# Kernel optimization log

Hardware: AMD Instinct MI355X
Metric: run time of the kernel (lower is better)

Reference implementation:

```python
import jax, jax.numpy as jnp
import numpy as np

B, L, C = 16, 2048, 128
FACTOR = 5
EPS = 1e-5


def setup_inputs() -> dict:
    key = jax.random.key(0)
    ks = jax.random.split(key, 16)
    U = min(FACTOR * int(np.ceil(np.log(L))), L)  # U_part == u == 40 for L=2048
    inp = {"x": jax.random.normal(ks[0], (B, L, C), jnp.float32)}
    scalar_names = ["Wq", "bq", "Wk", "bk", "Wv", "bv", "Wo", "bo", "w1", "b1", "w2", "b2"]
    for i, n in enumerate(scalar_names):
        inp[n] = jax.random.normal(ks[i + 1], (1,), jnp.float32) * 0.5
    inp["g1"] = jnp.ones((1,), jnp.float32)
    inp["beta1"] = jnp.zeros((1,), jnp.float32)
    inp["g2"] = jnp.ones((1,), jnp.float32)
    inp["beta2"] = jnp.zeros((1,), jnp.float32)
    # ProbAttention's random key-sampling indices (torch.randint(L_K, (L_Q, sample_k)))
    inp["index_sample"] = jax.random.randint(ks[14], (L, U), 0, L, dtype=jnp.int32)
    return inp


def _layernorm(x, g, b):
    # norm_dims=2 with d_model=1: normalize jointly over (seq_len, 1) == seq axis here
    m = x.mean(-1, keepdims=True)
    v = x.var(-1, keepdims=True)
    return (x - m) * jax.lax.rsqrt(v + EPS) * g + b


def reference(x, Wq, bq, Wk, bk, Wv, bv, Wo, bo, w1, b1, w2, b2,
              g1, beta1, g2, beta2, index_sample):
    U = index_sample.shape[1]  # sample_k == n_top (L_Q == L_K)
    batch_idx = jnp.arange(B)[:, None]

    def chan(xc):  # xc: [B, L] one channel, d_model=1 squeezed (H=1, D=1 -> scale=1)
        q = xc * Wq + bq
        k = xc * Wk + bk
        v = xc * Wv + bv
        # sparse measurement: sample U keys per query
        K_s = k[:, index_sample]                      # [B, L, U]
        QK = q[:, :, None] * K_s                      # [B, L, U]
        M = QK.max(-1) - QK.sum(-1) / L               # [B, L]
        _, M_top = jax.lax.top_k(M, U)                # [B, U] top-u query indices
        Qr = jnp.take_along_axis(q, M_top, axis=1)    # [B, U]
        scores = Qr[:, :, None] * k[:, None, :]       # [B, U, L], scale = 1/sqrt(1)
        attn = jax.nn.softmax(scores, axis=-1)
        upd = jnp.einsum('bul,bl->bu', attn, v)       # [B, U]
        # initial context = mean of V (mask_flag=False), updated at top queries
        ctx = jnp.broadcast_to(v.mean(1, keepdims=True), xc.shape)
        ctx = ctx.at[batch_idx, M_top].set(upd)       # [B, L]
        new_x = ctx * Wo + bo                          # out_projection
        x1 = _layernorm(xc + new_x, g1, beta1)
        y = jax.nn.gelu(x1 * w1 + b1, approximate=False)  # conv1 (1x1, 1->1) + gelu
        y = y * w2 + b2                                    # conv2 (1x1, 1->1)
        return _layernorm(x1 + y, g2, beta2)

    # all cfg.d_model encoder layers share one weight set -> vmap over channels
    return jax.vmap(chan, in_axes=2, out_axes=2)(x)  # [B, L, C]
```

## Files before the change

kernel.cpp:

```cpp
#include <hip/hip_runtime.h>
#include <math.h>

#define LL 2048
#define CC 128
#define BB 16
#define UU 40
#define NT 256
#define NW 4
#define EPSF 1e-5f

__device__ __forceinline__ float waveSum(float v) {
#pragma unroll
    for (int off = 1; off < 64; off <<= 1) v += __shfl_xor(v, off, 64);
    return v;
}
__device__ __forceinline__ float waveMax(float v) {
#pragma unroll
    for (int off = 1; off < 64; off <<= 1) v = fmaxf(v, __shfl_xor(v, off, 64));
    return v;
}
__device__ __forceinline__ float waveMin(float v) {
#pragma unroll
    for (int off = 1; off < 64; off <<= 1) v = fminf(v, __shfl_xor(v, off, 64));
    return v;
}
__device__ __forceinline__ float blockSum(float v, volatile float* scr) {
    v = waveSum(v);
    const int lane = threadIdx.x & 63, wid = threadIdx.x >> 6;
    __syncthreads();
    if (lane == 0) scr[wid] = v;
    __syncthreads();
    return scr[0] + scr[1] + scr[2] + scr[3];
}
__device__ __forceinline__ float blockMax(float v, volatile float* scr) {
    v = waveMax(v);
    const int lane = threadIdx.x & 63, wid = threadIdx.x >> 6;
    __syncthreads();
    if (lane == 0) scr[wid] = v;
    __syncthreads();
    return fmaxf(fmaxf(scr[0], scr[1]), fmaxf(scr[2], scr[3]));
}
__device__ __forceinline__ float blockMin(float v, volatile float* scr) {
    v = waveMin(v);
    const int lane = threadIdx.x & 63, wid = threadIdx.x >> 6;
    __syncthreads();
    if (lane == 0) scr[wid] = v;
    __syncthreads();
    return fminf(fminf(scr[0], scr[1]), fminf(scr[2], scr[3]));
}

__global__ __launch_bounds__(256) void transpose_dual(
    const float* __restrict__ x,  float* __restrict__ xT,
    const float* __restrict__ M,  float* __restrict__ MT) {
    __shared__ float t[32][33];
    const int z  = blockIdx.z;
    const int b  = (z < BB) ? z : (z - BB);
    const float* in  = (z < BB) ? x  : M;
    float* outp      = (z < BB) ? xT : MT;
    const int c0 = blockIdx.x * 32, l0 = blockIdx.y * 32;
    const int lx = threadIdx.x, ly = threadIdx.y;
    const float* base = in + ((size_t)b * LL + l0) * CC + c0;
#pragma unroll
    for (int i = 0; i < 4; ++i) t[ly + i * 8][lx] = base[(size_t)(ly + i * 8) * CC + lx];
    __syncthreads();
    float* obase = outp + ((size_t)b * CC + c0) * LL + l0;
#pragma unroll
    for (int i = 0; i < 4; ++i) obase[(size_t)(ly + i * 8) * LL + lx] = t[lx][ly + i * 8];
}
__global__ __launch_bounds__(256) void transpose_out(const float* __restrict__ in,
                                                     float* __restrict__ outp) {
    __shared__ float t[32][33];
    const int b  = blockIdx.z;
    const int l0 = blockIdx.x * 32, c0 = blockIdx.y * 32;
    const int lx = threadIdx.x, ly = threadIdx.y;
    const float* base = in + ((size_t)b * CC + c0) * LL + l0;
#pragma unroll
    for (int i = 0; i < 4; ++i) t[ly + i * 8][lx] = base[(size_t)(ly + i * 8) * LL + lx];
    __syncthreads();
    float* obase = outp + ((size_t)b * LL + l0) * CC + c0;
#pragma unroll
    for (int i = 0; i < 4; ++i) obase[(size_t)(ly + i * 8) * CC + lx] = t[lx][ly + i * 8];
}

__global__ __launch_bounds__(256) void agg_kernel(
    const float* __restrict__ x, const int* __restrict__ idx,
    const float* __restrict__ gWq, const float* __restrict__ gbq,
    const float* __restrict__ gWk, const float* __restrict__ gbk,
    float* __restrict__ M)
{
    __shared__ int s_idx[8 * UU];
    const int tid = threadIdx.x;
    const int g   = blockIdx.x;
    const int b   = ((g & 7) << 1) | ((g >> 3) & 1);
    const int l0  = (g >> 4) * 8;
    if (tid < 256)          s_idx[tid]       = idx[l0 * UU + tid];
    if (tid < 8 * UU - 256) s_idx[256 + tid] = idx[l0 * UU + 256 + tid];
    __syncthreads();

    const int s = tid & 31;
    const int r = tid >> 5;
    const int l = l0 + r;
    const float Wq = *gWq, bq = *gbq, Wk = *gWk, bk = *gbk;

    const float4* xb = (const float4*)(x + (size_t)b * LL * CC);
    float4 xo4 = xb[(size_t)l * 32 + s];
    float xo[4] = {xo4.x, xo4.y, xo4.z, xo4.w};

    float  mx[4] = {-3.4e38f, -3.4e38f, -3.4e38f, -3.4e38f};
    float  mn[4] = { 3.4e38f,  3.4e38f,  3.4e38f,  3.4e38f};
    double sm[4] = {0.0, 0.0, 0.0, 0.0};
    const int* rowp = &s_idx[r * UU];
#pragma unroll 8
    for (int u = 0; u < UU; ++u) {
        const int i = rowp[u];
        float4 xv = xb[(size_t)i * 32 + s];
        float xa[4] = {xv.x, xv.y, xv.z, xv.w};
#pragma unroll
        for (int t = 0; t < 4; ++t) {
            mx[t] = fmaxf(mx[t], xa[t]);
            mn[t] = fminf(mn[t], xa[t]);
            sm[t] += (double)xa[t];
        }
    }
    float mo[4];
#pragma unroll
    for (int t = 0; t < 4; ++t) {
        const float xH = (Wk >= 0.f) ? mx[t] : mn[t];
        const float xL = (Wk >= 0.f) ? mn[t] : mx[t];
        const float kH = __fadd_rn(__fmul_rn(xH, Wk), bk);
        const float kL = __fadd_rn(__fmul_rn(xL, Wk), bk);
        const float q  = __fadd_rn(__fmul_rn(xo[t], Wq), bq);
        const float t1 = __fmul_rn(q, (q >= 0.f) ? kH : kL);
        const double ks = (double)Wk * sm[t] + 40.0 * (double)bk;
        const float t2 = (float)(((double)q * ks) * (1.0 / 2048.0));
        mo[t] = __fsub_rn(t1, t2);
    }
    float4 Mo = make_float4(mo[0], mo[1], mo[2], mo[3]);
    ((float4*)(M + ((size_t)b * LL + l) * CC))[s] = Mo;
}

__global__ __launch_bounds__(NT) void rowBC(
    const float* __restrict__ xT,
    float* MoT,
    const float* __restrict__ gWq, const float* __restrict__ gbq,
    const float* __restrict__ gWk, const float* __restrict__ gbk,
    const float* __restrict__ gWv, const float* __restrict__ gbv,
    const float* __restrict__ gWo, const float* __restrict__ gbo,
    const float* __restrict__ gw1, const float* __restrict__ gb1,
    const float* __restrict__ gw2, const float* __restrict__ gb2,
    const float* __restrict__ gg1, const float* __restrict__ gbe1,
    const float* __restrict__ gg2, const float* __restrict__ gbe2)
{
    const int tid = threadIdx.x;
    const int ln  = tid & 63;
    const int wid = tid >> 6;
    const int r   = blockIdx.x * 4 + wid;

    __shared__ __align__(16) float s_ctx[4][LL];
    __shared__ int s_top[4][UU];

    const float Wq = *gWq, bq = *gbq, Wk = *gWk, bk = *gbk;
    const float Wv = *gWv, bv = *gbv, Wo = *gWo, bo = *gbo;
    const float w1 = *gw1, b1 = *gb1, w2 = *gw2, b2 = *gb2;
    const float g1 = *gg1, be1 = *gbe1, g2 = *gg2, be2 = *gbe2;

    const float*  xrow  = xT + (size_t)r * LL;
    const float4* xrow4 = (const float4*)xrow;
    float* Mrow = MoT + (size_t)r * LL;
    const float4* mrow4 = (const float4*)Mrow;
    float4* orow4 = (float4*)Mrow;
    float4* lds4  = (float4*)s_ctx[wid];

    float4 mv[8];
#pragma unroll
    for (int m = 0; m < 8; ++m) mv[m] = mrow4[ln + m * 64];

    float bvv = -3.4e38f; int bii = LL + 1;
#pragma unroll
    for (int m = 0; m < 8; ++m) {
        const int l0 = 4 * (ln + 64 * m);
        if (mv[m].x > bvv) { bvv = mv[m].x; bii = l0; }
        if (mv[m].y > bvv) { bvv = mv[m].y; bii = l0 + 1; }
        if (mv[m].z > bvv) { bvv = mv[m].z; bii = l0 + 2; }
        if (mv[m].w > bvv) { bvv = mv[m].w; bii = l0 + 3; }
    }
    for (int t = 0; t < UU; ++t) {
        float rv = bvv; int ri = bii;
#pragma unroll
        for (int off = 1; off < 64; off <<= 1) {
            float ov = __shfl_xor(rv, off, 64);
            int   oi = __shfl_xor(ri, off, 64);
            if (ov > rv || (ov == rv && oi < ri)) { rv = ov; ri = oi; }
        }
        if (ln == 0) s_top[wid][t] = ri;
        if (bii == ri) {
#pragma unroll
            for (int m = 0; m < 8; ++m) {
                const int l0 = 4 * (ln + 64 * m);
                if (l0     == ri) mv[m].x = -3.4e38f;
                if (l0 + 1 == ri) mv[m].y = -3.4e38f;
                if (l0 + 2 == ri) mv[m].z = -3.4e38f;
                if (l0 + 3 == ri) mv[m].w = -3.4e38f;
            }
            bvv = -3.4e38f; bii = LL + 1;
#pragma unroll
            for (int m = 0; m < 8; ++m) {
                const int l0 = 4 * (ln + 64 * m);
                if (mv[m].x > bvv) { bvv = mv[m].x; bii = l0; }
                if (mv[m].y > bvv) { bvv = mv[m].y; bii = l0 + 1; }
                if (mv[m].z > bvv) { bvv = mv[m].z; bii = l0 + 2; }
                if (mv[m].w > bvv) { bvv = mv[m].w; bii = l0 + 3; }
            }
        }
    }

    float4 xc[8];
    float vsum = 0.f, xmx = -3.4e38f, xmn = 3.4e38f;
#pragma unroll
    for (int m = 0; m < 8; ++m) {
        float4 xv = xrow4[ln + m * 64];
        xc[m] = xv;
        vsum += __fadd_rn(__fmul_rn(xv.x, Wv), bv) + __fadd_rn(__fmul_rn(xv.y, Wv), bv)
              + __fadd_rn(__fmul_rn(xv.z, Wv), bv) + __fadd_rn(__fmul_rn(xv.w, Wv), bv);
        xmx = fmaxf(xmx, fmaxf(fmaxf(xv.x, xv.y), fmaxf(xv.z, xv.w)));
        xmn = fminf(xmn, fminf(fminf(xv.x, xv.y), fminf(xv.z, xv.w)));
    }
    vsum = waveSum(vsum);
    xmx  = waveMax(xmx);
    xmn  = waveMin(xmn);
    const float vmean = vsum * (1.f / (float)LL);
    const float kmx = __fadd_rn(__fmul_rn((Wk >= 0.f) ? xmx : xmn, Wk), bk);
    const float kmn = __fadd_rn(__fmul_rn((Wk >= 0.f) ? xmn : xmx, Wk), bk);

#pragma unroll
    for (int m = 0; m < 8; ++m)
        lds4[ln + m * 64] = make_float4(vmean, vmean, vmean, vmean);

    for (int g = 0; g < UU / 4; ++g) {
        int p[4]; float qp[4], sm[4];
#pragma unroll
        for (int q = 0; q < 4; ++q) {
            p[q] = s_top[wid][g * 4 + q];
            const float xq = xrow[p[q]];
            qp[q] = __fadd_rn(__fmul_rn(xq, Wq), bq);
            sm[q] = (qp[q] >= 0.f) ? __fmul_rn(qp[q], kmx) : __fmul_rn(qp[q], kmn);
        }
        float se[4] = {0.f, 0.f, 0.f, 0.f};
        float sx[4] = {0.f, 0.f, 0.f, 0.f};
#pragma unroll
        for (int m = 0; m < 8; ++m) {
            float4 x4 = xc[m];
            float4 k4;
            k4.x = __fadd_rn(__fmul_rn(x4.x, Wk), bk);
            k4.y = __fadd_rn(__fmul_rn(x4.y, Wk), bk);
            k4.z = __fadd_rn(__fmul_rn(x4.z, Wk), bk);
            k4.w = __fadd_rn(__fmul_rn(x4.w, Wk), bk);
#pragma unroll
            for (int q = 0; q < 4; ++q) {
                float e;
                e = __expf(fmaf(qp[q], k4.x, -sm[q])); se[q] += e; sx[q] = fmaf(e, x4.x, sx[q]);
                e = __expf(fmaf(qp[q], k4.y, -sm[q])); se[q] += e; sx[q] = fmaf(e, x4.y, sx[q]);
                e = __expf(fmaf(qp[q], k4.z, -sm[q])); se[q] += e; sx[q] = fmaf(e, x4.z, sx[q]);
                e = __expf(fmaf(qp[q], k4.w, -sm[q])); se[q] += e; sx[q] = fmaf(e, x4.w, sx[q]);
            }
        }
#pragma unroll
        for (int q = 0; q < 4; ++q) {
            const float seA = waveSum(se[q]);
            const float sxA = waveSum(sx[q]);
            const float upd = (Wv * sxA + bv * seA) / seA;
            if (ln == 0) s_ctx[wid][p[q]] = upd;
        }
    }

    float4 tt[8];
    float lsum = 0.f;
#pragma unroll
    for (int m = 0; m < 8; ++m) {
        float4 cx = lds4[ln + m * 64], xv = xc[m], tv;
        tv.x = xv.x + __fadd_rn(__fmul_rn(cx.x, Wo), bo);
        tv.y = xv.y + __fadd_rn(__fmul_rn(cx.y, Wo), bo);
        tv.z = xv.z + __fadd_rn(__fmul_rn(cx.z, Wo), bo);
        tv.w = xv.w + __fadd_rn(__fmul_rn(cx.w, Wo), bo);
        tt[m] = tv;
        lsum += tv.x + tv.y + tv.z + tv.w;
    }
    const float mean1 = waveSum(lsum) * (1.f / (float)LL);
    float lss = 0.f;
#pragma unroll
    for (int m = 0; m < 8; ++m) {
        float4 tv = tt[m];
        float d0 = tv.x - mean1, d1 = tv.y - mean1, d2 = tv.z - mean1, d3 = tv.w - mean1;
        lss += d0 * d0 + d1 * d1 + d2 * d2 + d3 * d3;
    }
    const float var1 = waveSum(lss) * (1.f / (float)LL);
    const float rs1 = rsqrtf(var1 + EPSF);

    float lsum2 = 0.f;
#pragma unroll
    for (int m = 0; m < 8; ++m) {
        float4 tv = tt[m], zz;
        {
            float x1 = (tv.x - mean1) * rs1 * g1 + be1;
            float a = x1 * w1 + b1;
            float y = 0.5f * a * (1.f + erff(a * 0.70710678118654752f));
            zz.x = x1 + (y * w2 + b2);
        }
        {
            float x1 = (tv.y - mean1) * rs1 * g1 + be1;
            float a = x1 * w1 + b1;
            float y = 0.5f * a * (1.f + erff(a * 0.70710678118654752f));
            zz.y = x1 + (y * w2 + b2);
        }
        {
            float x1 = (tv.z - mean1) * rs1 * g1 + be1;
            float a = x1 * w1 + b1;
            float y = 0.5f * a * (1.f + erff(a * 0.70710678118654752f));
            zz.z = x1 + (y * w2 + b2);
        }
        {
            float x1 = (tv.w - mean1) * rs1 * g1 + be1;
            float a = x1 * w1 + b1;
            float y = 0.5f * a * (1.f + erff(a * 0.70710678118654752f));
            zz.w = x1 + (y * w2 + b2);
        }
        tt[m] = zz;
        lsum2 += zz.x + zz.y + zz.z + zz.w;
    }
    const float mean2 = waveSum(lsum2) * (1.f / (float)LL);
    float lss2 = 0.f;
#pragma unroll
    for (int m = 0; m < 8; ++m) {
        float4 zz = tt[m];
        float d0 = zz.x - mean2, d1 = zz.y - mean2, d2 = zz.z - mean2, d3 = zz.w - mean2;
        lss2 += d0 * d0 + d1 * d1 + d2 * d2 + d3 * d3;
    }
    const float var2 = waveSum(lss2) * (1.f / (float)LL);
    const float rs2 = rsqrtf(var2 + EPSF);

#pragma unroll
    for (int m = 0; m < 8; ++m) {
        float4 zz = tt[m], oo;
        oo.x = (zz.x - mean2) * rs2 * g2 + be2;
        oo.y = (zz.y - mean2) * rs2 * g2 + be2;
        oo.z = (zz.z - mean2) * rs2 * g2 + be2;
        oo.w = (zz.w - mean2) * rs2 * g2 + be2;
        orow4[ln + m * 64] = oo;
    }
}

__global__ __launch_bounds__(NT) void informer_fallback(
    const float* __restrict__ xin,
    const float* __restrict__ gWq, const float* __restrict__ gbq,
    const float* __restrict__ gWk, const float* __restrict__ gbk,
    const float* __restrict__ gWv, const float* __restrict__ gbv,
    const float* __restrict__ gWo, const float* __restrict__ gbo,
    const float* __restrict__ gw1, const float* __restrict__ gb1,
    const float* __restrict__ gw2, const float* __restrict__ gb2,
    const float* __restrict__ gg1, const float* __restrict__ gbe1,
    const float* __restrict__ gg2, const float* __restrict__ gbe2,
    const int* __restrict__ idx,
    float* __restrict__ outp)
{
    const int tid  = threadIdx.x;
    const int lane = tid & 63;
    const int wid  = tid >> 6;
    const int blk  = blockIdx.x;
    const int b    = blk >> 7;
    const int c    = blk & (CC - 1);

    __shared__ float  s_xc[LL];
    __shared__ float  s_kc[LL];
    __shared__ float  s_v[LL];
    __shared__ float  s_red[NW];
    __shared__ double s_cv[NW * UU];
    __shared__ int    s_ci[NW * UU];
    __shared__ int    s_top[UU];
    __shared__ float  s_upd[UU];

    const float Wq = *gWq, bq = *gbq, Wk = *gWk, bk = *gbk;
    const float Wv = *gWv, bv = *gbv, Wo = *gWo, bo = *gbo;
    const float w1 = *gw1, b1 = *gb1, w2 = *gw2, b2 = *gb2;
    const float g1 = *gg1, be1 = *gbe1, g2 = *gg2, be2 = *gbe2;

    const float* xrow = xin + (size_t)b * LL * CC + c;
    float* orow = outp + (size_t)b * LL * CC + c;

    float vsum = 0.f, kmn = 3.4e38f, kmx = -3.4e38f;
    for (int l = tid; l < LL; l += NT) {
        float xv = xrow[(size_t)l * CC];
        s_xc[l] = xv;
        float kvv = __fadd_rn(__fmul_rn(xv, Wk), bk);
        float vvv = __fadd_rn(__fmul_rn(xv, Wv), bv);
        s_kc[l] = kvv;
        s_v[l] = vvv;
        vsum += vvv;
        kmn = fminf(kmn, kvv);
        kmx = fmaxf(kmx, kvv);
    }
    const float vmean  = blockSum(vsum, s_red) * (1.f / (float)LL);
    const float kmxAll = blockMax(kmx, s_red);
    const float kmnAll = blockMin(kmn, s_red);

    double mloc[8];
#pragma unroll
    for (int j = 0; j < 8; ++j) {
        const int l = tid + NT * j;
        const float qv = __fadd_rn(__fmul_rn(s_xc[l], Wq), bq);
        const double qd = (double)qv;
        const int* row = idx + l * UU;
        float kmaxs = -3.4e38f, kmins = 3.4e38f;
        double ssum = 0.0;
#pragma unroll 8
        for (int u = 0; u < UU; ++u) {
            float kvv = s_kc[row[u]];
            kmaxs = fmaxf(kmaxs, kvv);
            kmins = fminf(kmins, kvv);
            ssum += (double)kvv;
        }
        double qmax = (qd >= 0.0) ? qd * (double)kmaxs : qd * (double)kmins;
        mloc[j] = qmax - qd * ssum * (1.0 / (double)LL);
    }

    double wbv = mloc[0]; int wbi = tid;
#pragma unroll
    for (int j = 1; j < 8; ++j)
        if (mloc[j] > wbv) { wbv = mloc[j]; wbi = tid + NT * j; }

    for (int t = 0; t < UU; ++t) {
        double rv = wbv; int ri = wbi;
#pragma unroll
        for (int off = 1; off < 64; off <<= 1) {
            double ov = __shfl_xor(rv, off, 64);
            int    oi = __shfl_xor(ri, off, 64);
            if (ov > rv || (ov == rv && oi < ri)) { rv = ov; ri = oi; }
        }
        if (lane == 0) { s_cv[wid * UU + t] = rv; s_ci[wid * UU + t] = ri; }
        if (wbi == ri) {
#pragma unroll
            for (int j = 0; j < 8; ++j) if ((tid + NT * j) == ri) mloc[j] = -1e300;
            wbv = mloc[0]; wbi = tid;
#pragma unroll
            for (int j = 1; j < 8; ++j)
                if (mloc[j] > wbv) { wbv = mloc[j]; wbi = tid + NT * j; }
        }
    }
    __syncthreads();

    if (wid == 0) {
        double c0v = s_cv[lane], c1v = s_cv[lane + 64];
        int    c0i = s_ci[lane], c1i = s_ci[lane + 64];
        double c2v = (lane < 32) ? s_cv[lane + 128] : -1e300;
        int    c2i = (lane < 32) ? s_ci[lane + 128] : (LL + 1);
        for (int t = 0; t < UU; ++t) {
            double rv = c0v; int ri = c0i;
            if (c1v > rv || (c1v == rv && c1i < ri)) { rv = c1v; ri = c1i; }
            if (c2v > rv || (c2v == rv && c2i < ri)) { rv = c2v; ri = c2i; }
#pragma unroll
            for (int off = 1; off < 64; off <<= 1) {
                double ov = __shfl_xor(rv, off, 64);
                int    oi = __shfl_xor(ri, off, 64);
                if (ov > rv || (ov == rv && oi < ri)) { rv = ov; ri = oi; }
            }
            if (lane == 0) s_top[t] = ri;
            if (c0i == ri) c0v = -1e300;
            else if (c1i == ri) c1v = -1e300;
            else if (c2i == ri) c2v = -1e300;
        }
    }
    __syncthreads();

    for (int r = 0; r < UU / NW; ++r) {
        const int u = r * NW + wid;
        const int p = s_top[u];
        const float qp = __fadd_rn(__fmul_rn(s_xc[p], Wq), bq);
        const float smax = (qp >= 0.f) ? qp * kmxAll : qp * kmnAll;
        float se = 0.f, sev = 0.f;
        for (int l = lane; l < LL; l += 64) {
            float e = __expf(qp * s_kc[l] - smax);
            se += e;
            sev = fmaf(e, s_v[l], sev);
        }
        se = waveSum(se); sev = waveSum(sev);
        if (lane == 0) s_upd[u] = sev / se;
    }
    __syncthreads();

    for (int l = tid; l < LL; l += NT) s_kc[l] = vmean;
    __syncthreads();
    if (tid < UU) s_kc[s_top[tid]] = s_upd[tid];
    __syncthreads();

    float lsum = 0.f;
    for (int l = tid; l < LL; l += NT) {
        float tv = s_xc[l] + __fadd_rn(__fmul_rn(s_kc[l], Wo), bo);
        s_kc[l] = tv;
        lsum += tv;
    }
    const float mean1 = blockSum(lsum, s_red) * (1.f / (float)LL);
    float lss = 0.f;
    for (int l = tid; l < LL; l += NT) { float d = s_kc[l] - mean1; lss += d * d; }
    const float var1 = blockSum(lss, s_red) * (1.f / (float)LL);
    const float rs1 = rsqrtf(var1 + EPSF);

    float lsum2 = 0.f;
    for (int l = tid; l < LL; l += NT) {
        float x1 = (s_kc[l] - mean1) * rs1 * g1 + be1;
        float a  = x1 * w1 + b1;
        float y  = 0.5f * a * (1.f + erff(a * 0.70710678118654752f));
        y = y * w2 + b2;
        float z = x1 + y;
        s_kc[l] = z;
        lsum2 += z;
    }
    const float mean2 = blockSum(lsum2, s_red) * (1.f / (float)LL);
    float lss2 = 0.f;
    for (int l = tid; l < LL; l += NT) { float d = s_kc[l] - mean2; lss2 += d * d; }
    const float var2 = blockSum(lss2, s_red) * (1.f / (float)LL);
    const float rs2 = rsqrtf(var2 + EPSF);

    for (int l = tid; l < LL; l += NT)
        orow[(size_t)l * CC] = (s_kc[l] - mean2) * rs2 * g2 + be2;
}

extern "C" void kernel_launch(void* const* d_in, const int* in_sizes, int n_in,
                              void* d_out, int out_size, void* d_ws, size_t ws_size,
                              hipStream_t stream) {
    const float* x   = (const float*)d_in[0];
    const float* Wq  = (const float*)d_in[1];
    const float* bq  = (const float*)d_in[2];
    const float* Wk  = (const float*)d_in[3];
    const float* bk  = (const float*)d_in[4];
    const float* Wv  = (const float*)d_in[5];
    const float* bv  = (const float*)d_in[6];
    const float* Wo  = (const float*)d_in[7];
    const float* bo  = (const float*)d_in[8];
    const float* w1  = (const float*)d_in[9];
    const float* b1  = (const float*)d_in[10];
    const float* w2  = (const float*)d_in[11];
    const float* b2  = (const float*)d_in[12];
    const float* g1  = (const float*)d_in[13];
    const float* be1 = (const float*)d_in[14];
    const float* g2  = (const float*)d_in[15];
    const float* be2 = (const float*)d_in[16];
    const int*   idx = (const int*)d_in[17];
    float* out = (float*)d_out;

    const size_t SZ = (size_t)BB * LL * CC * sizeof(float);

    if (ws_size >= 2 * SZ) {
        float* xT = (float*)d_ws;
        float* MT = (float*)((char*)d_ws + SZ);
        agg_kernel<<<dim3((LL / 8) * BB), dim3(256), 0, stream>>>(x, idx, Wq, bq, Wk, bk, out);
        transpose_dual<<<dim3(CC / 32, LL / 32, 2 * BB), dim3(32, 8), 0, stream>>>(x, xT, out, MT);
        rowBC<<<dim3(BB * CC / 4), dim3(NT), 0, stream>>>(
            xT, MT, Wq, bq, Wk, bk, Wv, bv, Wo, bo, w1, b1, w2, b2,
            g1, be1, g2, be2);
        transpose_out<<<dim3(LL / 32, CC / 32, BB), dim3(32, 8), 0, stream>>>(MT, out);
    } else {
        informer_fallback<<<dim3(BB * CC), dim3(NT), 0, stream>>>(
            x, Wq, bq, Wk, bk, Wv, bv, Wo, bo, w1, b1, w2, b2,
            g1, be1, g2, be2, idx, out);
    }
}
```

Measured before the change: 235.0 us.

## Split each row across a block's four waves and fold k-projection into exp2

```diff
diff --git a/kernel.cpp b/kernel.cpp
--- a/kernel.cpp
+++ b/kernel.cpp
@@ -154,22 +154,24 @@
     const int tid = threadIdx.x;
     const int ln  = tid & 63;
     const int wid = tid >> 6;
-    const int r   = blockIdx.x * 4 + wid;
-
-    __shared__ __align__(16) float s_ctx[4][LL];
-    __shared__ int s_top[4][UU];
+    const int r   = blockIdx.x;
+
+    __shared__ __align__(16) float s_ctx[LL];
+    __shared__ int   s_top[UU];
+    __shared__ float s_red[NW];
 
     const float Wq = *gWq, bq = *gbq, Wk = *gWk, bk = *gbk;
     const float Wv = *gWv, bv = *gbv, Wo = *gWo, bo = *gbo;
     const float w1 = *gw1, b1 = *gb1, w2 = *gw2, b2 = *gb2;
     const float g1 = *gg1, be1 = *gbe1, g2 = *gg2, be2 = *gbe2;
+    const float LOG2E = 1.4426950408889634f;
 
     const float*  xrow  = xT + (size_t)r * LL;
     const float4* xrow4 = (const float4*)xrow;
     float* Mrow = MoT + (size_t)r * LL;
     const float4* mrow4 = (const float4*)Mrow;
     float4* orow4 = (float4*)Mrow;
-    float4* lds4  = (float4*)s_ctx[wid];
+    float4* ctx4  = (float4*)s_ctx;
 
     float4 mv[8];
 #pragma unroll
@@ -192,7 +194,7 @@
             int   oi = __shfl_xor(ri, off, 64);
             if (ov > rv || (ov == rv && oi < ri)) { rv = ov; ri = oi; }
         }
-        if (ln == 0) s_top[wid][t] = ri;
+        if (ln == 0) s_top[t] = ri;
         if (bii == ri) {
 #pragma unroll
             for (int m = 0; m < 8; ++m) {
@@ -232,121 +234,106 @@
     const float kmx = __fadd_rn(__fmul_rn((Wk >= 0.f) ? xmx : xmn, Wk), bk);
     const float kmn = __fadd_rn(__fmul_rn((Wk >= 0.f) ? xmn : xmx, Wk), bk);
 
-#pragma unroll
-    for (int m = 0; m < 8; ++m)
-        lds4[ln + m * 64] = make_float4(vmean, vmean, vmean, vmean);
-
-    for (int g = 0; g < UU / 4; ++g) {
-        int p[4]; float qp[4], sm[4];
-#pragma unroll
-        for (int q = 0; q < 4; ++q) {
-            p[q] = s_top[wid][g * 4 + q];
+    const float4 vm4 = make_float4(vmean, vmean, vmean, vmean);
+    ctx4[128 * wid + ln]      = vm4;
+    ctx4[128 * wid + 64 + ln] = vm4;
+    __syncthreads();
+
+#pragma unroll
+    for (int g = 0; g < 2; ++g) {
+        int p[5]; float A[5], Bc[5];
+#pragma unroll
+        for (int q = 0; q < 5; ++q) {
+            p[q] = s_top[wid * 10 + g * 5 + q];
             const float xq = xrow[p[q]];
-            qp[q] = __fadd_rn(__fmul_rn(xq, Wq), bq);
-            sm[q] = (qp[q] >= 0.f) ? __fmul_rn(qp[q], kmx) : __fmul_rn(qp[q], kmn);
-        }
-        float se[4] = {0.f, 0.f, 0.f, 0.f};
-        float sx[4] = {0.f, 0.f, 0.f, 0.f};
+            const float qp = __fadd_rn(__fmul_rn(xq, Wq), bq);
+            const float sm = (qp >= 0.f) ? __fmul_rn(qp, kmx) : __fmul_rn(qp, kmn);
+            A[q]  = qp * Wk * LOG2E;
+            Bc[q] = (qp * bk - sm) * LOG2E;
+        }
+        float se[5] = {0.f, 0.f, 0.f, 0.f, 0.f};
+        float sx[5] = {0.f, 0.f, 0.f, 0.f, 0.f};
 #pragma unroll
         for (int m = 0; m < 8; ++m) {
             float4 x4 = xc[m];
-            float4 k4;
-            k4.x = __fadd_rn(__fmul_rn(x4.x, Wk), bk);
-            k4.y = __fadd_rn(__fmul_rn(x4.y, Wk), bk);
-            k4.z = __fadd_rn(__fmul_rn(x4.z, Wk), bk);
-            k4.w = __fadd_rn(__fmul_rn(x4.w, Wk), bk);
-#pragma unroll
-            for (int q = 0; q < 4; ++q) {
+#pragma unroll
+            for (int q = 0; q < 5; ++q) {
                 float e;
-                e = __expf(fmaf(qp[q], k4.x, -sm[q])); se[q] += e; sx[q] = fmaf(e, x4.x, sx[q]);
-                e = __expf(fmaf(qp[q], k4.y, -sm[q])); se[q] += e; sx[q] = fmaf(e, x4.y, sx[q]);
-                e = __expf(fmaf(qp[q], k4.z, -sm[q])); se[q] += e; sx[q] = fmaf(e, x4.z, sx[q]);
-                e = __expf(fmaf(qp[q], k4.w, -sm[q])); se[q] += e; sx[q] = fmaf(e, x4.w, sx[q]);
+                e = exp2f(fmaf(A[q], x4.x, Bc[q])); se[q] += e; sx[q] = fmaf(e, x4.x, sx[q]);
+                e = exp2f(fmaf(A[q], x4.y, Bc[q])); se[q] += e; sx[q] = fmaf(e, x4.y, sx[q]);
+                e = exp2f(fmaf(A[q], x4.z, Bc[q])); se[q] += e; sx[q] = fmaf(e, x4.z, sx[q]);
+                e = exp2f(fmaf(A[q], x4.w, Bc[q])); se[q] += e; sx[q] = fmaf(e, x4.w, sx[q]);
             }
         }
 #pragma unroll
-        for (int q = 0; q < 4; ++q) {
+        for (int q = 0; q < 5; ++q) {
             const float seA = waveSum(se[q]);
             const float sxA = waveSum(sx[q]);
             const float upd = (Wv * sxA + bv * seA) / seA;
-            if (ln == 0) s_ctx[wid][p[q]] = upd;
-        }
-    }
-
-    float4 tt[8];
-    float lsum = 0.f;
-#pragma unroll
-    for (int m = 0; m < 8; ++m) {
-        float4 cx = lds4[ln + m * 64], xv = xc[m], tv;
-        tv.x = xv.x + __fadd_rn(__fmul_rn(cx.x, Wo), bo);
-        tv.y = xv.y + __fadd_rn(__fmul_rn(cx.y, Wo), bo);
-        tv.z = xv.z + __fadd_rn(__fmul_rn(cx.z, Wo), bo);
-        tv.w = xv.w + __fadd_rn(__fmul_rn(cx.w, Wo), bo);
-        tt[m] = tv;
-        lsum += tv.x + tv.y + tv.z + tv.w;
-    }
-    const float mean1 = waveSum(lsum) * (1.f / (float)LL);
+            if (ln == 0) s_ctx[p[q]] = upd;
+        }
+    }
+    __syncthreads();
+
+    const int f0 = 128 * wid + ln, f1 = f0 + 64;
+    float4 xa = xrow4[f0], xb = xrow4[f1];
+    float4 ca = ctx4[f0],  cb = ctx4[f1];
+    float4 ta, tb;
+    ta.x = xa.x + __fadd_rn(__fmul_rn(ca.x, Wo), bo);
+    ta.y = xa.y + __fadd_rn(__fmul_rn(ca.y, Wo), bo);
+    ta.z = xa.z + __fadd_rn(__fmul_rn(ca.z, Wo), bo);
+    ta.w = xa.w + __fadd_rn(__fmul_rn(ca.w, Wo), bo);
+    tb.x = xb.x + __fadd_rn(__fmul_rn(cb.x, Wo), bo);
+    tb.y = xb.y + __fadd_rn(__fmul_rn(cb.y, Wo), bo);
+    tb.z = xb.z + __fadd_rn(__fmul_rn(cb.z, Wo), bo);
+    tb.w = xb.w + __fadd_rn(__fmul_rn(cb.w, Wo), bo);
+    float lsum = ta.x + ta.y + ta.z + ta.w + tb.x + tb.y + tb.z + tb.w;
+    const float mean1 = blockSum(lsum, s_red) * (1.f / (float)LL);
     float lss = 0.f;
-#pragma unroll
-    for (int m = 0; m < 8; ++m) {
-        float4 tv = tt[m];
-        float d0 = tv.x - mean1, d1 = tv.y - mean1, d2 = tv.z - mean1, d3 = tv.w - mean1;
-        lss += d0 * d0 + d1 * d1 + d2 * d2 + d3 * d3;
-    }
-    const float var1 = waveSum(lss) * (1.f / (float)LL);
+    {
+        float d0 = ta.x - mean1, d1 = ta.y - mean1, d2 = ta.z - mean1, d3 = ta.w - mean1;
+        float d4 = tb.x - mean1, d5 = tb.y - mean1, d6 = tb.z - mean1, d7 = tb.w - mean1;
+        lss = d0*d0 + d1*d1 + d2*d2 + d3*d3 + d4*d4 + d5*d5 + d6*d6 + d7*d7;
+    }
+    const float var1 = blockSum(lss, s_red) * (1.f / (float)LL);
     const float rs1 = rsqrtf(var1 + EPSF);
 
-    float lsum2 = 0.f;
-#pragma unroll
-    for (int m = 0; m < 8; ++m) {
-        float4 tv = tt[m], zz;
-        {
-            float x1 = (tv.x - mean1) * rs1 * g1 + be1;
-            float a = x1 * w1 + b1;
-            float y = 0.5f * a * (1.f + erff(a * 0.70710678118654752f));
-            zz.x = x1 + (y * w2 + b2);
-        }
-        {
-            float x1 = (tv.y - mean1) * rs1 * g1 + be1;
-            float a = x1 * w1 + b1;
-            float y = 0.5f * a * (1.f + erff(a * 0.70710678118654752f));
-            zz.y = x1 + (y * w2 + b2);
-        }
-        {
-            float x1 = (tv.z - mean1) * rs1 * g1 + be1;
-            float a = x1 * w1 + b1;
-            float y = 0.5f * a * (1.f + erff(a * 0.70710678118654752f));
-            zz.z = x1 + (y * w2 + b2);
-        }
-        {
-            float x1 = (tv.w - mean1) * rs1 * g1 + be1;
-            float a = x1 * w1 + b1;
-            float y = 0.5f * a * (1.f + erff(a * 0.70710678118654752f));
-            zz.w = x1 + (y * w2 + b2);
-        }
-        tt[m] = zz;
-        lsum2 += zz.x + zz.y + zz.z + zz.w;
-    }
-    const float mean2 = waveSum(lsum2) * (1.f / (float)LL);
+    float za[4], zb[4];
+    {
+        const float tin[8] = {ta.x, ta.y, ta.z, ta.w, tb.x, tb.y, tb.z, tb.w};
+        float zo[8];
+#pragma unroll
+        for (int e = 0; e < 8; ++e) {
+            float x1 = (tin[e] - mean1) * rs1 * g1 + be1;
+            float a  = x1 * w1 + b1;
+            float y  = 0.5f * a * (1.f + erff(a * 0.70710678118654752f));
+            zo[e] = x1 + (y * w2 + b2);
+        }
+        za[0] = zo[0]; za[1] = zo[1]; za[2] = zo[2]; za[3] = zo[3];
+        zb[0] = zo[4]; zb[1] = zo[5]; zb[2] = zo[6]; zb[3] = zo[7];
+    }
+    float lsum2 = za[0] + za[1] + za[2] + za[3] + zb[0] + zb[1] + zb[2] + zb[3];
+    const float mean2 = blockSum(lsum2, s_red) * (1.f / (float)LL);
     float lss2 = 0.f;
 #pragma unroll
-    for (int m = 0; m < 8; ++m) {
-        float4 zz = tt[m];
-        float d0 = zz.x - mean2, d1 = zz.y - mean2, d2 = zz.z - mean2, d3 = zz.w - mean2;
-        lss2 += d0 * d0 + d1 * d1 + d2 * d2 + d3 * d3;
-    }
-    const float var2 = waveSum(lss2) * (1.f / (float)LL);
+    for (int e = 0; e < 4; ++e) {
+        float d0 = za[e] - mean2, d1 = zb[e] - mean2;
+        lss2 += d0 * d0 + d1 * d1;
+    }
+    const float var2 = blockSum(lss2, s_red) * (1.f / (float)LL);
     const float rs2 = rsqrtf(var2 + EPSF);
 
-#pragma unroll
-    for (int m = 0; m < 8; ++m) {
-        float4 zz = tt[m], oo;
-        oo.x = (zz.x - mean2) * rs2 * g2 + be2;
-        oo.y = (zz.y - mean2) * rs2 * g2 + be2;
-        oo.z = (zz.z - mean2) * rs2 * g2 + be2;
-        oo.w = (zz.w - mean2) * rs2 * g2 + be2;
-        orow4[ln + m * 64] = oo;
-    }
+    float4 oa, ob;
+    oa.x = (za[0] - mean2) * rs2 * g2 + be2;
+    oa.y = (za[1] - mean2) * rs2 * g2 + be2;
+    oa.z = (za[2] - mean2) * rs2 * g2 + be2;
+    oa.w = (za[3] - mean2) * rs2 * g2 + be2;
+    ob.x = (zb[0] - mean2) * rs2 * g2 + be2;
+    ob.y = (zb[1] - mean2) * rs2 * g2 + be2;
+    ob.z = (zb[2] - mean2) * rs2 * g2 + be2;
+    ob.w = (zb[3] - mean2) * rs2 * g2 + be2;
+    orow4[f0] = oa;
+    orow4[f1] = ob;
 }
 
 __global__ __launch_bounds__(NT) void informer_fallback(
@@ -553,7 +540,7 @@
         float* MT = (float*)((char*)d_ws + SZ);
         agg_kernel<<<dim3((LL / 8) * BB), dim3(256), 0, stream>>>(x, idx, Wq, bq, Wk, bk, out);
         transpose_dual<<<dim3(CC / 32, LL / 32, 2 * BB), dim3(32, 8), 0, stream>>>(x, xT, out, MT);
-        rowBC<<<dim3(BB * CC / 4), dim3(NT), 0, stream>>>(
+        rowBC<<<dim3(BB * CC), dim3(NT), 0, stream>>>(
             xT, MT, Wq, bq, Wk, bk, Wv, bv, Wo, bo, w1, b1, w2, b2,
             g1, be1, g2, be2);
         transpose_out<<<dim3(LL / 32, CC / 32, BB), dim3(32, 8), 0, stream>>>(MT, out);
```

After: 299.8 us. 1.28x slower.

## Use per-lane top-4 cache for top-k selection and fold key affine into exp2

Applied to the files above, without the earlier changes.

```diff
diff --git a/kernel.cpp b/kernel.cpp
--- a/kernel.cpp
+++ b/kernel.cpp
@@ -138,6 +138,18 @@
     float4 Mo = make_float4(mo[0], mo[1], mo[2], mo[3]);
     ((float4*)(M + ((size_t)b * LL + l) * CC))[s] = Mo;
 }
+
+#define TOP4_INSERT(val, idxl)                                                  \
+    {                                                                           \
+        const bool b0 = (val) > cv0 || ((val) == cv0 && (idxl) < ci0);          \
+        const bool b1 = (val) > cv1 || ((val) == cv1 && (idxl) < ci1);          \
+        const bool b2 = (val) > cv2 || ((val) == cv2 && (idxl) < ci2);          \
+        const bool b3 = (val) > cv3 || ((val) == cv3 && (idxl) < ci3);          \
+        if (b0)      { cv3=cv2;ci3=ci2; cv2=cv1;ci2=ci1; cv1=cv0;ci1=ci0; cv0=(val);ci0=(idxl); } \
+        else if (b1) { cv3=cv2;ci3=ci2; cv2=cv1;ci2=ci1; cv1=(val);ci1=(idxl); } \
+        else if (b2) { cv3=cv2;ci3=ci2; cv2=(val);ci2=(idxl); }                 \
+        else if (b3) { cv3=(val);ci3=(idxl); }                                  \
+    }
 
 __global__ __launch_bounds__(NT) void rowBC(
     const float* __restrict__ xT,
@@ -163,6 +175,7 @@
     const float Wv = *gWv, bv = *gbv, Wo = *gWo, bo = *gbo;
     const float w1 = *gw1, b1 = *gb1, w2 = *gw2, b2 = *gb2;
     const float g1 = *gg1, be1 = *gbe1, g2 = *gg2, be2 = *gbe2;
+    const float LOG2E = 1.4426950408889634f;
 
     const float*  xrow  = xT + (size_t)r * LL;
     const float4* xrow4 = (const float4*)xrow;
@@ -171,45 +184,47 @@
     float4* orow4 = (float4*)Mrow;
     float4* lds4  = (float4*)s_ctx[wid];
 
-    float4 mv[8];
-#pragma unroll
-    for (int m = 0; m < 8; ++m) mv[m] = mrow4[ln + m * 64];
-
-    float bvv = -3.4e38f; int bii = LL + 1;
-#pragma unroll
-    for (int m = 0; m < 8; ++m) {
-        const int l0 = 4 * (ln + 64 * m);
-        if (mv[m].x > bvv) { bvv = mv[m].x; bii = l0; }
-        if (mv[m].y > bvv) { bvv = mv[m].y; bii = l0 + 1; }
-        if (mv[m].z > bvv) { bvv = mv[m].z; bii = l0 + 2; }
-        if (mv[m].w > bvv) { bvv = mv[m].w; bii = l0 + 3; }
-    }
-    for (int t = 0; t < UU; ++t) {
-        float rv = bvv; int ri = bii;
-#pragma unroll
-        for (int off = 1; off < 64; off <<= 1) {
-            float ov = __shfl_xor(rv, off, 64);
-            int   oi = __shfl_xor(ri, off, 64);
-            if (ov > rv || (ov == rv && oi < ri)) { rv = ov; ri = oi; }
-        }
-        if (ln == 0) s_top[wid][t] = ri;
-        if (bii == ri) {
-#pragma unroll
-            for (int m = 0; m < 8; ++m) {
-                const int l0 = 4 * (ln + 64 * m);
-                if (l0     == ri) mv[m].x = -3.4e38f;
-                if (l0 + 1 == ri) mv[m].y = -3.4e38f;
-                if (l0 + 2 == ri) mv[m].z = -3.4e38f;
-                if (l0 + 3 == ri) mv[m].w = -3.4e38f;
+    {
+        float cv0 = -3.4e38f, cv1 = -3.4e38f, cv2 = -3.4e38f, cv3 = -3.4e38f;
+        int   ci0 = LL + 1,   ci1 = LL + 1,   ci2 = LL + 1,   ci3 = LL + 1;
+#pragma unroll
+        for (int m = 0; m < 8; ++m) {
+            float4 w = mrow4[ln + m * 64];
+            const int l0 = 4 * (ln + 64 * m);
+            TOP4_INSERT(w.x, l0);
+            TOP4_INSERT(w.y, l0 + 1);
+            TOP4_INSERT(w.z, l0 + 2);
+            TOP4_INSERT(w.w, l0 + 3);
+        }
+        unsigned int consumed = 0u;
+        for (int t = 0; t < UU; ++t) {
+            float rv = cv0; int ri = ci0;
+#pragma unroll
+            for (int off = 1; off < 64; off <<= 1) {
+                float ov = __shfl_xor(rv, off, 64);
+                int   oi = __shfl_xor(ri, off, 64);
+                if (ov > rv || (ov == rv && oi < ri)) { rv = ov; ri = oi; }
             }
-            bvv = -3.4e38f; bii = LL + 1;
-#pragma unroll
-            for (int m = 0; m < 8; ++m) {
-                const int l0 = 4 * (ln + 64 * m);
-                if (mv[m].x > bvv) { bvv = mv[m].x; bii = l0; }
-                if (mv[m].y > bvv) { bvv = mv[m].y; bii = l0 + 1; }
-                if (mv[m].z > bvv) { bvv = mv[m].z; bii = l0 + 2; }
-                if (mv[m].w > bvv) { bvv = mv[m].w; bii = l0 + 3; }
+            if (ln == 0) s_top[wid][t] = ri;
+            if (ci0 == ri) {
+                const int qq = ri & 3;
+                const int mm = ((ri >> 2) - ln) >> 6;
+                consumed |= (1u << (4 * mm + qq));
+                cv0 = cv1; ci0 = ci1; cv1 = cv2; ci1 = ci2;
+                cv2 = cv3; ci2 = ci3; cv3 = -3.4e38f; ci3 = LL + 1;
+                if (ci0 == LL + 1) {
+                    cv0 = cv1 = cv2 = cv3 = -3.4e38f;
+                    ci0 = ci1 = ci2 = ci3 = LL + 1;
+#pragma unroll
+                    for (int m = 0; m < 8; ++m) {
+                        float4 w = mrow4[ln + m * 64];
+                        const int l0 = 4 * (ln + 64 * m);
+                        if (!(consumed & (1u << (4 * m + 0)))) TOP4_INSERT(w.x, l0);
+                        if (!(consumed & (1u << (4 * m + 1)))) TOP4_INSERT(w.y, l0 + 1);
+                        if (!(consumed & (1u << (4 * m + 2)))) TOP4_INSERT(w.z, l0 + 2);
+                        if (!(consumed & (1u << (4 * m + 3)))) TOP4_INSERT(w.w, l0 + 3);
+                    }
+                }
             }
         }
     }
@@ -237,31 +252,28 @@
         lds4[ln + m * 64] = make_float4(vmean, vmean, vmean, vmean);
 
     for (int g = 0; g < UU / 4; ++g) {
-        int p[4]; float qp[4], sm[4];
+        int p[4]; float A[4], Bc[4];
 #pragma unroll
         for (int q = 0; q < 4; ++q) {
             p[q] = s_top[wid][g * 4 + q];
             const float xq = xrow[p[q]];
-            qp[q] = __fadd_rn(__fmul_rn(xq, Wq), bq);
-            sm[q] = (qp[q] >= 0.f) ? __fmul_rn(qp[q], kmx) : __fmul_rn(qp[q], kmn);
+            const float qp = __fadd_rn(__fmul_rn(xq, Wq), bq);
+            const float sm = (qp >= 0.f) ? __fmul_rn(qp, kmx) : __fmul_rn(qp, kmn);
+            A[q]  = qp * Wk * LOG2E;
+            Bc[q] = (qp * bk - sm) * LOG2E;
         }
         float se[4] = {0.f, 0.f, 0.f, 0.f};
         float sx[4] = {0.f, 0.f, 0.f, 0.f};
 #pragma unroll
         for (int m = 0; m < 8; ++m) {
             float4 x4 = xc[m];
-            float4 k4;
-            k4.x = __fadd_rn(__fmul_rn(x4.x, Wk), bk);
-            k4.y = __fadd_rn(__fmul_rn(x4.y, Wk), bk);
-            k4.z = __fadd_rn(__fmul_rn(x4.z, Wk), bk);
-            k4.w = __fadd_rn(__fmul_rn(x4.w, Wk), bk);
 #pragma unroll
             for (int q = 0; q < 4; ++q) {
                 float e;
-                e = __expf(fmaf(qp[q], k4.x, -sm[q])); se[q] += e; sx[q] = fmaf(e, x4.x, sx[q]);
-                e = __expf(fmaf(qp[q], k4.y, -sm[q])); se[q] += e; sx[q] = fmaf(e, x4.y, sx[q]);
-                e = __expf(fmaf(qp[q], k4.z, -sm[q])); se[q] += e; sx[q] = fmaf(e, x4.z, sx[q]);
-                e = __expf(fmaf(qp[q], k4.w, -sm[q])); se[q] += e; sx[q] = fmaf(e, x4.w, sx[q]);
+                e = exp2f(fmaf(A[q], x4.x, Bc[q])); se[q] += e; sx[q] = fmaf(e, x4.x, sx[q]);
+                e = exp2f(fmaf(A[q], x4.y, Bc[q])); se[q] += e; sx[q] = fmaf(e, x4.y, sx[q]);
+                e = exp2f(fmaf(A[q], x4.z, Bc[q])); se[q] += e; sx[q] = fmaf(e, x4.z, sx[q]);
+                e = exp2f(fmaf(A[q], x4.w, Bc[q])); se[q] += e; sx[q] = fmaf(e, x4.w, sx[q]);
             }
         }
 #pragma unroll
```

Measured after the change: 248.2 us. +5.6%, slower.
